# Performance work log

Measured on AMD Instinct MI355X. Metric: run time of the kernel, lower is better.

## Reference

```python
import jax, jax.numpy as jnp
import numpy as np

V = 32000; D = 512; H = 8; DH = D // H; L = 12; E = 8; FF = 2048
B = 2; S = 1024; MAXPOS = 2048
EPS = 1e-6; NEG = -1e9


def _rmsnorm(x, w):
    return x * jax.lax.rsqrt(jnp.mean(x * x, axis=-1, keepdims=True) + EPS) * w


def setup_inputs() -> dict:
    key = jax.random.key(0)
    ks = jax.random.split(key, 10)
    s = 0.02
    n = lambda k, shp: jax.random.normal(k, shp, jnp.float32) * s
    return {
        "input_ids": jax.random.randint(ks[0], (B, S), 0, V),
        "tok_emb": n(ks[1], (V, D)),
        "pos_emb": n(ks[2], (MAXPOS, D)),
        "Wqkv": n(ks[3], (L, D, 3 * D)), "bqkv": jnp.zeros((L, 3 * D), jnp.float32),
        "Wo": n(ks[4], (L, D, D)), "bo": jnp.zeros((L, D), jnp.float32),
        "rW": n(ks[5], (L, D, E)), "rb": jnp.zeros((L, E), jnp.float32),
        "eW1": n(ks[6], (L, E, D, FF)), "eb1": jnp.zeros((L, E, FF), jnp.float32),
        "eW2": n(ks[7], (L, E, FF, D)), "eb2": jnp.zeros((L, E, D), jnp.float32),
        "n1w": jnp.ones((L, D), jnp.float32), "n2w": jnp.ones((L, D), jnp.float32),
        "now": jnp.ones((D,), jnp.float32), "lmW": n(ks[8], (D, V)),
    }


def _forward(input_ids, tok_emb, pos_emb, Wqkv, bqkv, Wo, bo, rW, rb,
             eW1, eb1, eW2, eb2, n1w, n2w, now, lmW):
    x = tok_emb[input_ids] + pos_emb[:S]              # [B,S,D]
    causal = jnp.tril(jnp.ones((S, S), bool))         # lower-triangular mask

    def step(x, p):
        wqkv, bq, wo, bo_, rw, rb_, w1, b1, w2, b2, g1, g2 = p
        # --- causal self-attention ---
        h = _rmsnorm(x, g1)
        qkv = h @ wqkv + bq
        q, k, v = [t.reshape(B, S, H, DH) for t in jnp.split(qkv, 3, axis=-1)]
        scores = jnp.einsum('bqhd,bkhd->bhqk', q, k) / jnp.sqrt(jnp.float32(DH))
        scores = jnp.where(causal, scores, NEG)
        attn = jax.nn.softmax(scores, axis=-1)
        o = jnp.einsum('bhqk,bkhd->bqhd', attn, v).reshape(B, S, D) @ wo + bo_
        x = x + o
        # --- MoE layer, top-1 routing ---
        h = _rmsnorm(x, g2)
        rl = h @ rw + rb_                              # router logits [B,S,E]
        probs = jax.nn.softmax(rl, axis=-1)
        top_w = jnp.max(probs, axis=-1)                # top-1 gate weight [B,S]
        top_i = jnp.argmax(probs, axis=-1)             # expert id [B,S]
        one_hot = jax.nn.one_hot(top_i, E, dtype=x.dtype)
        frac = jnp.mean(one_hot, axis=(0, 1))          # fraction of tokens per expert
        pmean = jnp.mean(probs, axis=(0, 1))           # mean router prob per expert
        aux = E * jnp.sum(frac * pmean)                # switch-style load-balance loss
        disp = (one_hot * top_w[..., None]).reshape(-1, E)   # [T,E] weighted dispatch
        hf = h.reshape(-1, D)                          # [T,D]
        hid = jax.nn.gelu(jnp.einsum('td,edf->etf', hf, w1) + b1[:, None, :], approximate=False)
        outs = jnp.einsum('etf,efd->etd', hid, w2) + b2[:, None, :]
        y = jnp.einsum('etd,te->td', outs, disp).reshape(B, S, D)  # scatter-combine
        x = x + y
        return x, (aux, rl)

    x, (auxes, rlogits) = jax.lax.scan(
        step, x, (Wqkv, bqkv, Wo, bo, rW, rb, eW1, eb1, eW2, eb2, n1w, n2w))
    logits = _rmsnorm(x, now) @ lmW                    # [B,S,V]
    return logits, jnp.sum(auxes), rlogits


def reference(input_ids, tok_emb, pos_emb, Wqkv, bqkv, Wo, bo, rW, rb,
              eW1, eb1, eW2, eb2, n1w, n2w, now, lmW):
    return _forward(input_ids, tok_emb, pos_emb, Wqkv, bqkv, Wo, bo, rW, rb,
                    eW1, eb1, eW2, eb2, n1w, n2w, now, lmW)
```

## Files before the change

kernel.cpp:

```cpp
#include <hip/hip_runtime.h>

constexpr int B_  = 2, S_ = 1024, T_ = 2048;
constexpr int D_  = 512, H_ = 8, DH_ = 64;
constexpr int L_  = 12, E_ = 8, FF_ = 2048;
constexpr int V_  = 32000, D3_ = 1536;

using half8_t = __attribute__((ext_vector_type(8))) _Float16;
using half2_t = __attribute__((ext_vector_type(2))) _Float16;
using f32x4_t = __attribute__((ext_vector_type(4))) float;

__device__ __forceinline__ float wred(float v){
#pragma unroll
  for (int off = 32; off; off >>= 1) v += __shfl_xor(v, off);
  return v;
}
__device__ __forceinline__ float gelu_f(float v){
  return 0.5f * v * (1.f + erff(v * 0.70710678118654752f));
}

__global__ void k_embed(const int* __restrict__ ids, const float* __restrict__ tok,
                        const float* __restrict__ pos, float* __restrict__ x){
  int t = blockIdx.x;
  int s = t & (S_ - 1);
  int id = ids[t];
  const float* tr = tok + (size_t)id * D_;
  const float* pr = pos + (size_t)s  * D_;
  float* xr = x + (size_t)t * D_;
  for (int d = threadIdx.x; d < D_; d += blockDim.x) xr[d] = tr[d] + pr[d];
}

__global__ __launch_bounds__(64) void k_norm_router(
    const float* __restrict__ x, const float* __restrict__ nw,
    const float* __restrict__ rW, const float* __restrict__ rb,
    float* __restrict__ h, float* __restrict__ rl_out,
    float* __restrict__ topw, int* __restrict__ topi){
  const int t = blockIdx.x, lane = threadIdx.x;
  const float* xr = x + (size_t)t * D_;
  const float4 xv0 = *reinterpret_cast<const float4*>(xr + (lane << 2));
  const float4 xv1 = *reinterpret_cast<const float4*>(xr + 256 + (lane << 2));
  float ss = xv0.x*xv0.x + xv0.y*xv0.y + xv0.z*xv0.z + xv0.w*xv0.w
           + xv1.x*xv1.x + xv1.y*xv1.y + xv1.z*xv1.z + xv1.w*xv1.w;
  ss = wred(ss);
  const float sc = rsqrtf(ss * (1.f / (float)D_) + 1e-6f);
  const float4 w0 = *reinterpret_cast<const float4*>(nw + (lane << 2));
  const float4 w1 = *reinterpret_cast<const float4*>(nw + 256 + (lane << 2));
  float hv[8];
  hv[0] = xv0.x*sc*w0.x; hv[1] = xv0.y*sc*w0.y; hv[2] = xv0.z*sc*w0.z; hv[3] = xv0.w*sc*w0.w;
  hv[4] = xv1.x*sc*w1.x; hv[5] = xv1.y*sc*w1.y; hv[6] = xv1.z*sc*w1.z; hv[7] = xv1.w*sc*w1.w;
  float* hr = h + (size_t)t * D_;
  *reinterpret_cast<float4*>(hr + (lane << 2))       = make_float4(hv[0], hv[1], hv[2], hv[3]);
  *reinterpret_cast<float4*>(hr + 256 + (lane << 2)) = make_float4(hv[4], hv[5], hv[6], hv[7]);
  float acc[8] = {0,0,0,0,0,0,0,0};
#pragma unroll
  for (int u = 0; u < 8; u++){
    const int d = (u < 4) ? ((lane << 2) + u) : (256 + (lane << 2) + u - 4);
    const float4 ra = *reinterpret_cast<const float4*>(rW + (size_t)d * E_);
    const float4 rb4 = *reinterpret_cast<const float4*>(rW + (size_t)d * E_ + 4);
    acc[0] += hv[u]*ra.x;  acc[1] += hv[u]*ra.y;  acc[2] += hv[u]*ra.z;  acc[3] += hv[u]*ra.w;
    acc[4] += hv[u]*rb4.x; acc[5] += hv[u]*rb4.y; acc[6] += hv[u]*rb4.z; acc[7] += hv[u]*rb4.w;
  }
  float rl[8];
#pragma unroll
  for (int e = 0; e < 8; e++) rl[e] = wred(acc[e]) + rb[e];
  float mx = rl[0];
#pragma unroll
  for (int e = 1; e < 8; e++) mx = fmaxf(mx, rl[e]);
  float p[8], s = 0.f;
#pragma unroll
  for (int e = 0; e < 8; e++){ p[e] = __expf(rl[e] - mx); s += p[e]; }
  const float inv = 1.f / s;
  int arg = 0; float best = rl[0];
#pragma unroll
  for (int e = 1; e < 8; e++) if (rl[e] > best){ best = rl[e]; arg = e; }
  if (lane == 0){
#pragma unroll
    for (int e = 0; e < 8; e++) rl_out[(size_t)t * E_ + e] = rl[e];
    topw[t] = p[arg] * inv;
    topi[t] = arg;
  }
}

__global__ __launch_bounds__(1024) void k_route_scan2(
    const int* __restrict__ topi, const float* __restrict__ rl,
    int* __restrict__ seg, int* __restrict__ perm, float* __restrict__ aux){
  __shared__ int cnt[8], segs[9], cur[8];
  __shared__ float psums[8];
  const int tid = threadIdx.x;
  if (tid < 8){ cnt[tid] = 0; psums[tid] = 0.f; }
  __syncthreads();
  const int t0 = tid, t1 = tid + 1024;
  const int e0 = topi[t0], e1 = topi[t1];
  atomicAdd(&cnt[e0], 1);
  atomicAdd(&cnt[e1], 1);
  float ps[8] = {0,0,0,0,0,0,0,0};
#pragma unroll
  for (int k = 0; k < 2; k++){
    const float* r = rl + (size_t)(k ? t1 : t0) * E_;
    float v[8];
#pragma unroll
    for (int e = 0; e < 8; e++) v[e] = r[e];
    float mx = v[0];
#pragma unroll
    for (int e = 1; e < 8; e++) mx = fmaxf(mx, v[e]);
    float s = 0.f;
#pragma unroll
    for (int e = 0; e < 8; e++){ v[e] = __expf(v[e] - mx); s += v[e]; }
    const float is = 1.f / s;
#pragma unroll
    for (int e = 0; e < 8; e++) ps[e] += v[e] * is;
  }
#pragma unroll
  for (int e = 0; e < 8; e++) ps[e] = wred(ps[e]);
  if ((tid & 63) == 0){
#pragma unroll
    for (int e = 0; e < 8; e++) atomicAdd(&psums[e], ps[e]);
  }
  __syncthreads();
  if (tid == 0){
    segs[0] = 0;
#pragma unroll
    for (int e = 0; e < 8; e++) segs[e + 1] = segs[e] + cnt[e];
#pragma unroll
    for (int e = 0; e < 8; e++) cur[e] = segs[e];
  }
  __syncthreads();
  if (tid < 9) seg[tid] = segs[tid];
  const int p0 = atomicAdd(&cur[e0], 1); perm[p0] = t0;
  const int p1 = atomicAdd(&cur[e1], 1); perm[p1] = t1;
  if (tid == 0){
    float av = 0.f;
#pragma unroll
    for (int e = 0; e < 8; e++) av += (float)cnt[e] * psums[e];
    aux[0] += 8.f * av * (1.f / ((float)T_ * (float)T_));
  }
}

template<int BM, int BN, int NPROD, int EPI, bool MOE, bool APERM, int SWZROWS, bool ANORM>
__global__ __launch_bounds__(256) void k_mgemm(
    const float* __restrict__ A, const float* __restrict__ Bm,
    const float* __restrict__ bias, float* __restrict__ C,
    int M, int N, int K,
    const int* __restrict__ seg, const int* __restrict__ perm,
    const float* __restrict__ topw, const float* __restrict__ nw){
  constexpr int FM = BM / 32, FN = BN / 32;
  const int tid = threadIdx.x;
  int rowTile, colTile;
  if (SWZROWS > 0){
    const int nwg = gridDim.x;
    const int bid = blockIdx.x;
    const int lb = (bid & 7) * (nwg >> 3) + (bid >> 3);
    rowTile = lb % SWZROWS;
    colTile = lb / SWZROWS;
  } else {
    colTile = blockIdx.x; rowTile = blockIdx.y;
  }
  int e = 0, s0 = 0, cnt = M;
  if (MOE){ e = blockIdx.z; s0 = seg[e]; cnt = seg[e + 1] - s0; }
  const int row0 = rowTile * BM, col0 = colTile * BN;
  if (MOE && row0 >= cnt) return;
  const float* Bp = Bm + (size_t)e * K * N;
  const float* bp = bias + (size_t)e * N;

  __shared__ __align__(16) _Float16 Ah[BM * 32];
  __shared__ __align__(16) _Float16 Al[NPROD == 3 ? BM * 32 : 8];
  __shared__ __align__(16) _Float16 Bh[BN * 32];
  __shared__ __align__(16) _Float16 Bl[NPROD == 3 ? BN * 32 : 8];

  const int am = (BM == 64) ? (tid >> 2) : (tid >> 1);
  const int agrow = row0 + am;
  const bool aval = agrow < cnt;
  const float* Arow = nullptr;
  if (aval){
    int ridx = APERM ? perm[s0 + agrow] : (MOE ? s0 + agrow : agrow);
    Arow = A + (size_t)ridx * K;
  }
  const int asub = am >> 4;
  const int cb = (BN == 128) ? ((tid & 31) << 2) : ((tid & 15) << 2);
  const int p0 = (BN == 128) ? (tid >> 5) : (tid >> 4);
  constexpr int NBI = (BN == 128) ? 2 : 1;

  const int lane = tid & 63, w = tid >> 6;
  const int wm0 = (w >> 1) * (BM / 2), wn0 = (w & 1) * (BN / 2);

  float ascale = 1.f;
  if (ANORM){
    float ss = 0.f;
    if (BM == 64){
      const int kg = tid & 3;
      for (int k0 = 0; k0 < K; k0 += 32){
        const float4 a0 = *reinterpret_cast<const float4*>(Arow + k0 + (kg << 3));
        const float4 a1 = *reinterpret_cast<const float4*>(Arow + k0 + (kg << 3) + 4);
        ss += a0.x*a0.x + a0.y*a0.y + a0.z*a0.z + a0.w*a0.w
            + a1.x*a1.x + a1.y*a1.y + a1.z*a1.z + a1.w*a1.w;
      }
      ss += __shfl_xor(ss, 1);
      ss += __shfl_xor(ss, 2);
    } else {
      const int kgb = (tid & 1) << 1;
      for (int k0 = 0; k0 < K; k0 += 32){
#pragma unroll
        for (int kq = 0; kq < 2; kq++){
          const int kg = kgb + kq;
          const float4 a0 = *reinterpret_cast<const float4*>(Arow + k0 + (kg << 3));
          const float4 a1 = *reinterpret_cast<const float4*>(Arow + k0 + (kg << 3) + 4);
          ss += a0.x*a0.x + a0.y*a0.y + a0.z*a0.z + a0.w*a0.w
              + a1.x*a1.x + a1.y*a1.y + a1.z*a1.z + a1.w*a1.w;
        }
      }
      ss += __shfl_xor(ss, 1);
    }
    ascale = rsqrtf(ss * (1.f / (float)K) + 1e-6f);
  }

  f32x4_t acc_hh[FM][FN];
  f32x4_t acc_mx[NPROD == 3 ? FM : 1][NPROD == 3 ? FN : 1];
#pragma unroll
  for (int i = 0; i < FM; i++)
#pragma unroll
    for (int j = 0; j < FN; j++){
      acc_hh[i][j] = (f32x4_t){0.f, 0.f, 0.f, 0.f};
      if (NPROD == 3) acc_mx[i][j] = (f32x4_t){0.f, 0.f, 0.f, 0.f};
    }

  for (int k0 = 0; k0 < K; k0 += 32){
    if (BM == 64){
      const int kg = tid & 3;
      float4 av0 = make_float4(0,0,0,0), av1 = make_float4(0,0,0,0);
      if (aval){
        av0 = *reinterpret_cast<const float4*>(Arow + k0 + (kg << 3));
        av1 = *reinterpret_cast<const float4*>(Arow + k0 + (kg << 3) + 4);
      }
      float a8[8] = {av0.x, av0.y, av0.z, av0.w, av1.x, av1.y, av1.z, av1.w};
      if (ANORM){
        const float4 w0 = *reinterpret_cast<const float4*>(nw + k0 + (kg << 3));
        const float4 w1 = *reinterpret_cast<const float4*>(nw + k0 + (kg << 3) + 4);
        const float wn8[8] = {w0.x, w0.y, w0.z, w0.w, w1.x, w1.y, w1.z, w1.w};
#pragma unroll
        for (int u = 0; u < 8; u++) a8[u] *= ascale * wn8[u];
      }
      half8_t hi, lo;
#pragma unroll
      for (int u = 0; u < 8; u++){
        hi[u] = (_Float16)a8[u];
        if (NPROD == 3) lo[u] = (_Float16)((a8[u] - (float)hi[u]) * 2048.f);
      }
      const int lidx = (am & 15) + (kg << 4);
      const int base = asub * 512 + ((lidx ^ (asub & 7)) << 3);
      *reinterpret_cast<half8_t*>(&Ah[base]) = hi;
      if (NPROD == 3) *reinterpret_cast<half8_t*>(&Al[base]) = lo;
    } else {
      const int kgb = (tid & 1) << 1;
#pragma unroll
      for (int kq = 0; kq < 2; kq++){
        const int kg = kgb + kq;
        float4 av0 = make_float4(0,0,0,0), av1 = make_float4(0,0,0,0);
        if (aval){
          av0 = *reinterpret_cast<const float4*>(Arow + k0 + (kg << 3));
          av1 = *reinterpret_cast<const float4*>(Arow + k0 + (kg << 3) + 4);
        }
        float a8[8] = {av0.x, av0.y, av0.z, av0.w, av1.x, av1.y, av1.z, av1.w};
        if (ANORM){
          const float4 w0 = *reinterpret_cast<const float4*>(nw + k0 + (kg << 3));
          const float4 w1 = *reinterpret_cast<const float4*>(nw + k0 + (kg << 3) + 4);
          const float wn8[8] = {w0.x, w0.y, w0.z, w0.w, w1.x, w1.y, w1.z, w1.w};
#pragma unroll
          for (int u = 0; u < 8; u++) a8[u] *= ascale * wn8[u];
        }
        half8_t hi;
#pragma unroll
        for (int u = 0; u < 8; u++) hi[u] = (_Float16)a8[u];
        const int lidx = (am & 15) + (kg << 4);
        *reinterpret_cast<half8_t*>(&Ah[asub * 512 + ((lidx ^ (asub & 7)) << 3)]) = hi;
      }
    }
#pragma unroll
    for (int it = 0; it < NBI; it++){
      const int kk = ((BN == 128) ? (p0 + (it << 3)) : p0) << 1;
      const int kg = kk >> 3, e2 = kk & 7;
      const float4 b0 = *reinterpret_cast<const float4*>(Bp + (size_t)(k0 + kk) * N + col0 + cb);
      const float4 b1 = *reinterpret_cast<const float4*>(Bp + (size_t)(k0 + kk + 1) * N + col0 + cb);
      const float b0a[4] = {b0.x, b0.y, b0.z, b0.w};
      const float b1a[4] = {b1.x, b1.y, b1.z, b1.w};
#pragma unroll
      for (int j = 0; j < 4; j++){
        const int c = cb + j, sub = c >> 4;
        const int lidx = (c & 15) + (kg << 4);
        const int base = sub * 512 + ((lidx ^ (sub & 7)) << 3) + e2;
        _Float16 h0 = (_Float16)b0a[j], h1 = (_Float16)b1a[j];
        *reinterpret_cast<half2_t*>(&Bh[base]) = (half2_t){h0, h1};
        if (NPROD == 3){
          _Float16 l0 = (_Float16)((b0a[j] - (float)h0) * 2048.f);
          _Float16 l1 = (_Float16)((b1a[j] - (float)h1) * 2048.f);
          *reinterpret_cast<half2_t*>(&Bl[base]) = (half2_t){l0, l1};
        }
      }
    }
    __syncthreads();
    half8_t fAh[FM], fBh[FN];
    half8_t fAl[NPROD == 3 ? FM : 1], fBl[NPROD == 3 ? FN : 1];
#pragma unroll
    for (int fm = 0; fm < FM; fm++){
      const int s = (wm0 >> 4) + fm;
      const int ofs = s * 512 + ((lane ^ (s & 7)) << 3);
      fAh[fm] = *reinterpret_cast<const half8_t*>(&Ah[ofs]);
      if (NPROD == 3) fAl[fm] = *reinterpret_cast<const half8_t*>(&Al[ofs]);
    }
#pragma unroll
    for (int fn = 0; fn < FN; fn++){
      const int s = (wn0 >> 4) + fn;
      const int ofs = s * 512 + ((lane ^ (s & 7)) << 3);
      fBh[fn] = *reinterpret_cast<const half8_t*>(&Bh[ofs]);
      if (NPROD == 3) fBl[fn] = *reinterpret_cast<const half8_t*>(&Bl[ofs]);
    }
#pragma unroll
    for (int fm = 0; fm < FM; fm++)
#pragma unroll
      for (int fn = 0; fn < FN; fn++){
        acc_hh[fm][fn] = __builtin_amdgcn_mfma_f32_16x16x32_f16(
            fAh[fm], fBh[fn], acc_hh[fm][fn], 0, 0, 0);
        if (NPROD == 3){
          acc_mx[fm][fn] = __builtin_amdgcn_mfma_f32_16x16x32_f16(
              fAh[fm], fBl[fn], acc_mx[fm][fn], 0, 0, 0);
          acc_mx[fm][fn] = __builtin_amdgcn_mfma_f32_16x16x32_f16(
              fAl[fm], fBh[fn], acc_mx[fm][fn], 0, 0, 0);
        }
      }
    __syncthreads();
  }

  const int lr = lane & 15, kg4 = lane >> 4;
#pragma unroll
  for (int fm = 0; fm < FM; fm++){
#pragma unroll
    for (int reg = 0; reg < 4; reg++){
      const int grow = row0 + wm0 + fm * 16 + (kg4 << 2) + reg;
      if (grow >= cnt) continue;
      int trow = 0; float tw = 0.f;
      if (EPI == 3){ trow = perm[s0 + grow]; tw = topw[trow]; }
#pragma unroll
      for (int fn = 0; fn < FN; fn++){
        const int col = col0 + wn0 + fn * 16 + lr;
        float v = acc_hh[fm][fn][reg];
        if (NPROD == 3) v += acc_mx[fm][fn][reg] * (1.f / 2048.f);
        if (EPI == 0){
          C[(size_t)grow * N + col] = v + bp[col];
        } else if (EPI == 1){
          C[(size_t)grow * N + col] += v + bp[col];
        } else if (EPI == 2){
          C[(size_t)(s0 + grow) * N + col] = gelu_f(v + bp[col]);
        } else if (EPI == 3){
          C[(size_t)trow * N + col] += tw * (v + bp[col]);
        } else {
          C[(size_t)grow * N + col] = v;
        }
      }
    }
  }
}

__global__ __launch_bounds__(256) void k_attn5(const float* __restrict__ qkv,
                                               float* __restrict__ o,
                                               float* __restrict__ attp,
                                               float* __restrict__ attml){
  __shared__ __align__(16) _Float16 Khi[4096], Klo[4096], Vhi[4096], Vlo[4096];
  __shared__ __align__(16) float pbuf[4][16 * 68];
  const int tid = threadIdx.x, w = tid >> 6, lane = tid & 63;
  const int lr = lane & 15, g = lane >> 4;
  const int bid = blockIdx.x;
  int bh, qt, kt0, kt1, mode;
  if (bid < 128){        bh = bid >> 3;            qt = 8 + (bid & 7);  kt0 = 0; kt1 = 7;  mode = 1; }
  else if (bid < 256){   const int j = bid - 128;  bh = j >> 3; qt = 7 - (j & 7);  kt0 = 0; kt1 = qt; mode = 0; }
  else {                 const int j = bid - 256;  bh = j >> 3; qt = 15 - (j & 7); kt0 = 8; kt1 = qt; mode = 2; }
  const int b = bh >> 3, h = bh & 7;
  const size_t bbase = (size_t)(b << 10) * D3_;
  const int hoff = h * 64;
  const int qg = (qt << 6) + (w << 4) + lr;

  half8_t qhi[2], qlo[2];
#pragma unroll
  for (int ks = 0; ks < 2; ks++){
    const float* qp = qkv + bbase + (size_t)qg * D3_ + hoff + ks * 32 + g * 8;
    const float4 f0 = *reinterpret_cast<const float4*>(qp);
    const float4 f1 = *reinterpret_cast<const float4*>(qp + 4);
    const float qa[8] = {f0.x, f0.y, f0.z, f0.w, f1.x, f1.y, f1.z, f1.w};
#pragma unroll
    for (int e = 0; e < 8; e++){
      const float v = qa[e] * 0.125f;
      const _Float16 hi = (_Float16)v;
      qhi[ks][e] = hi;
      qlo[ks][e] = (_Float16)((v - (float)hi) * 2048.f);
    }
  }

  float m = -1e30f, l = 0.f;
  f32x4_t oacc[4];
#pragma unroll
  for (int s = 0; s < 4; s++) oacc[s] = (f32x4_t){0.f, 0.f, 0.f, 0.f};

  const int kK = tid >> 2, quad = tid & 3;
  const int kp = tid >> 3, oct = tid & 7;

  float ka[16], va[8], vb[8];
  auto loadregs = [&](int kt){
    const int j0 = kt << 6;
    const float* kr = qkv + bbase + (size_t)(j0 + kK) * D3_ + 512 + hoff + quad * 16;
    const float4 f0 = *reinterpret_cast<const float4*>(kr);
    const float4 f1 = *reinterpret_cast<const float4*>(kr + 4);
    const float4 f2 = *reinterpret_cast<const float4*>(kr + 8);
    const float4 f3 = *reinterpret_cast<const float4*>(kr + 12);
    ka[0]=f0.x; ka[1]=f0.y; ka[2]=f0.z; ka[3]=f0.w;
    ka[4]=f1.x; ka[5]=f1.y; ka[6]=f1.z; ka[7]=f1.w;
    ka[8]=f2.x; ka[9]=f2.y; ka[10]=f2.z; ka[11]=f2.w;
    ka[12]=f3.x; ka[13]=f3.y; ka[14]=f3.z; ka[15]=f3.w;
    const int k0v = kp << 1;
    const float* vr = qkv + bbase + (size_t)(j0 + k0v) * D3_ + 1024 + hoff + oct * 8;
    const float4 a0 = *reinterpret_cast<const float4*>(vr);
    const float4 a1 = *reinterpret_cast<const float4*>(vr + 4);
    const float4 b0 = *reinterpret_cast<const float4*>(vr + D3_);
    const float4 b1 = *reinterpret_cast<const float4*>(vr + D3_ + 4);
    va[0]=a0.x; va[1]=a0.y; va[2]=a0.z; va[3]=a0.w;
    va[4]=a1.x; va[5]=a1.y; va[6]=a1.z; va[7]=a1.w;
    vb[0]=b0.x; vb[1]=b0.y; vb[2]=b0.z; vb[3]=b0.w;
    vb[4]=b1.x; vb[5]=b1.y; vb[6]=b1.z; vb[7]=b1.w;
  };
  auto writelds = [&](){
    const int ksd = quad >> 1;
#pragma unroll
    for (int ch = 0; ch < 2; ch++){
      const int kgd = ((quad << 1) + ch) & 3;
      const int base = ksd * 2048 + (kK >> 4) * 512 + (((kK & 15) + (kgd << 4)) << 3);
      half8_t hi, lo;
#pragma unroll
      for (int e = 0; e < 8; e++){
        const float v = ka[ch * 8 + e];
        const _Float16 hv = (_Float16)v;
        hi[e] = hv;
        lo[e] = (_Float16)((v - (float)hv) * 2048.f);
      }
      *reinterpret_cast<half8_t*>(&Khi[base]) = hi;
      *reinterpret_cast<half8_t*>(&Klo[base]) = lo;
    }
    const int ksk = kp >> 4, kgk = (kp >> 2) & 3, e0 = (kp & 3) << 1;
#pragma unroll
    for (int j = 0; j < 8; j++){
      const int d = oct * 8 + j;
      const int lidx = (d & 15) + (kgk << 4);
      const int sw = lidx ^ kgk ^ (ksk << 2);
      const int fa = ksk * 2048 + (d >> 4) * 512 + (sw << 3) + e0;
      const _Float16 h0 = (_Float16)va[j], h1 = (_Float16)vb[j];
      *reinterpret_cast<half2_t*>(&Vhi[fa]) = (half2_t){h0, h1};
      const _Float16 l0 = (_Float16)((va[j] - (float)h0) * 2048.f);
      const _Float16 l1 = (_Float16)((vb[j] - (float)h1) * 2048.f);
      *reinterpret_cast<half2_t*>(&Vlo[fa]) = (half2_t){l0, l1};
    }
  };

  loadregs(kt0);
  for (int kt = kt0; kt <= kt1; kt++){
    const int j0 = kt << 6;
    __syncthreads();
    writelds();
    if (kt < kt1) loadregs(kt + 1);
    __syncthreads();

    f32x4_t dfr[4];
#pragma unroll
    for (int s = 0; s < 4; s++){
      f32x4_t acc = (f32x4_t){0.f, 0.f, 0.f, 0.f};
      f32x4_t mix = (f32x4_t){0.f, 0.f, 0.f, 0.f};
#pragma unroll
      for (int ks = 0; ks < 2; ks++){
        const int base = ks * 2048 + s * 512 + lane * 8;
        const half8_t khi = *reinterpret_cast<const half8_t*>(&Khi[base]);
        const half8_t klo = *reinterpret_cast<const half8_t*>(&Klo[base]);
        acc = __builtin_amdgcn_mfma_f32_16x16x32_f16(khi, qhi[ks], acc, 0, 0, 0);
        mix = __builtin_amdgcn_mfma_f32_16x16x32_f16(khi, qlo[ks], mix, 0, 0, 0);
        mix = __builtin_amdgcn_mfma_f32_16x16x32_f16(klo, qhi[ks], mix, 0, 0, 0);
      }
#pragma unroll
      for (int r = 0; r < 4; r++) dfr[s][r] = acc[r] + mix[r] * (1.f / 2048.f);
    }
    if (kt == qt){
#pragma unroll
      for (int s = 0; s < 4; s++)
#pragma unroll
        for (int r = 0; r < 4; r++){
          const int keyg = j0 + (g << 2) + r + (s << 4);
          if (keyg > qg) dfr[s][r] = -1e30f;
        }
    }
    float mloc = dfr[0][0];
#pragma unroll
    for (int s = 0; s < 4; s++)
#pragma unroll
      for (int r = 0; r < 4; r++) mloc = fmaxf(mloc, dfr[s][r]);
    mloc = fmaxf(mloc, __shfl_xor(mloc, 16));
    mloc = fmaxf(mloc, __shfl_xor(mloc, 32));
    const float mn = fmaxf(m, mloc);
    const float cr = __expf(m - mn);
    float psum = 0.f;
#pragma unroll
    for (int s = 0; s < 4; s++)
#pragma unroll
      for (int r = 0; r < 4; r++){
        const float p = __expf(dfr[s][r] - mn);
        psum += p;
        pbuf[w][lr * 68 + (s << 4) + (g << 2) + r] = p;
      }
    psum += __shfl_xor(psum, 16);
    psum += __shfl_xor(psum, 32);
    l = l * cr + psum;
    m = mn;
#pragma unroll
    for (int s = 0; s < 4; s++)
#pragma unroll
      for (int r = 0; r < 4; r++) oacc[s][r] *= cr;

    half8_t phi[2], plo[2];
#pragma unroll
    for (int ks = 0; ks < 2; ks++){
      const float* pp = &pbuf[w][lr * 68 + ks * 32 + g * 8];
      const float4 p0 = *reinterpret_cast<const float4*>(pp);
      const float4 p1 = *reinterpret_cast<const float4*>(pp + 4);
      const float pa[8] = {p0.x,p0.y,p0.z,p0.w, p1.x,p1.y,p1.z,p1.w};
#pragma unroll
      for (int e = 0; e < 8; e++){
        const _Float16 hv = (_Float16)pa[e];
        phi[ks][e] = hv;
        plo[ks][e] = (_Float16)((pa[e] - (float)hv) * 2048.f);
      }
    }
#pragma unroll
    for (int s = 0; s < 4; s++){
      f32x4_t mix = (f32x4_t){0.f, 0.f, 0.f, 0.f};
#pragma unroll
      for (int ks = 0; ks < 2; ks++){
        const int sw = lane ^ g ^ (ks << 2);
        const int base = ks * 2048 + s * 512 + sw * 8;
        const half8_t vhi = *reinterpret_cast<const half8_t*>(&Vhi[base]);
        const half8_t vlo = *reinterpret_cast<const half8_t*>(&Vlo[base]);
        oacc[s] = __builtin_amdgcn_mfma_f32_16x16x32_f16(vhi, phi[ks], oacc[s], 0, 0, 0);
        mix = __builtin_amdgcn_mfma_f32_16x16x32_f16(vhi, plo[ks], mix, 0, 0, 0);
        mix = __builtin_amdgcn_mfma_f32_16x16x32_f16(vlo, phi[ks], mix, 0, 0, 0);
      }
#pragma unroll
      for (int r = 0; r < 4; r++) oacc[s][r] += mix[r] * (1.f / 2048.f);
    }
  }

  if (mode == 0){
    const float linv = 1.f / l;
    float* orow = o + (size_t)((b << 10) + qg) * D_ + hoff;
#pragma unroll
    for (int s = 0; s < 4; s++)
#pragma unroll
      for (int r = 0; r < 4; r++){
        const int d = (g << 2) + r + (s << 4);
        orow[d] = oacc[s][r] * linv;
      }
  } else {
    const int pidx = (((bh << 3) + (qt - 8)) << 1) + (mode - 1);
    float* pO = attp + (size_t)pidx * 4096;
    const int qloc = (w << 4) + lr;
#pragma unroll
    for (int s = 0; s < 4; s++)
#pragma unroll
      for (int r = 0; r < 4; r++){
        const int d = (g << 2) + r + (s << 4);
        pO[qloc * 64 + d] = oacc[s][r];
      }
    if (g == 0){
      attml[pidx * 128 + qloc]      = m;
      attml[pidx * 128 + 64 + qloc] = l;
    }
  }
}

__global__ __launch_bounds__(256) void k_attn_comb(const float* __restrict__ attp,
                                                   const float* __restrict__ attml,
                                                   float* __restrict__ o){
  const int bid = blockIdx.x;
  const int bh = bid >> 3, i = bid & 7, qt = 8 + i;
  const int b = bh >> 3, h = bh & 7;
  const int pidx0 = ((bh << 3) + i) << 1;
  const float* pA = attp + (size_t)pidx0 * 4096;
  const float* pB = pA + 4096;
  const float* mlA = attml + pidx0 * 128;
  const float* mlB = mlA + 128;
  const int tid = threadIdx.x;
  const int q = tid >> 2, dg = (tid & 3) << 4;
  const float mA = mlA[q], lA = mlA[64 + q];
  const float mB = mlB[q], lB = mlB[64 + q];
  const float M = fmaxf(mA, mB);
  const float cA = __expf(mA - M), cB = __expf(mB - M);
  const float linv = 1.f / (lA * cA + lB * cB);
  float* orow = o + (size_t)((b << 10) + (qt << 6) + q) * D_ + h * 64;
#pragma unroll
  for (int j = 0; j < 4; j++){
    const int d = dg + (j << 2);
    const float4 a = *reinterpret_cast<const float4*>(pA + q * 64 + d);
    const float4 bb = *reinterpret_cast<const float4*>(pB + q * 64 + d);
    *reinterpret_cast<float4*>(orow + d) = make_float4(
        (a.x * cA + bb.x * cB) * linv, (a.y * cA + bb.y * cB) * linv,
        (a.z * cA + bb.z * cB) * linv, (a.w * cA + bb.w * cB) * linv);
  }
}

extern "C" void kernel_launch(void* const* d_in, const int* in_sizes, int n_in,
                              void* d_out, int out_size, void* d_ws, size_t ws_size,
                              hipStream_t stream){
  const int*   ids  = (const int*)  d_in[0];
  const float* tok  = (const float*)d_in[1];
  const float* pos  = (const float*)d_in[2];
  const float* Wqkv = (const float*)d_in[3];
  const float* bqkv = (const float*)d_in[4];
  const float* Wo   = (const float*)d_in[5];
  const float* bo   = (const float*)d_in[6];
  const float* rW   = (const float*)d_in[7];
  const float* rb   = (const float*)d_in[8];
  const float* eW1  = (const float*)d_in[9];
  const float* eb1  = (const float*)d_in[10];
  const float* eW2  = (const float*)d_in[11];
  const float* eb2  = (const float*)d_in[12];
  const float* n1w  = (const float*)d_in[13];
  const float* n2w  = (const float*)d_in[14];
  const float* noww = (const float*)d_in[15];
  const float* lmW  = (const float*)d_in[16];

  float* out    = (float*)d_out;
  float* logits = out;
  float* aux    = out + (size_t)T_ * V_;
  float* rlog   = aux + 1;

  float* ws = (float*)d_ws;
  size_t off = 0;
  float* x     = ws + off; off += (size_t)T_ * D_;
  float* h     = ws + off; off += (size_t)T_ * D_;
  float* qkv   = ws + off; off += (size_t)T_ * D3_;
  float* attno = ws + off; off += (size_t)T_ * D_;
  float* hid   = ws + off; off += (size_t)T_ * FF_;
  float* topw  = ws + off; off += T_;
  int* topi    = (int*)(ws + off); off += T_;
  int* perm    = (int*)(ws + off); off += T_;
  int* seg     = (int*)(ws + off); off += (E_ + 1);
  float* attp  = ws + off; off += 16 * 8 * 2 * 4096;
  float* attml = ws + off; off += 16 * 8 * 2 * 128;

  hipMemsetAsync(aux, 0, sizeof(float), stream);
  k_embed<<<T_, 256, 0, stream>>>(ids, tok, pos, x);

  for (int l = 0; l < L_; l++){
    k_mgemm<64, 128, 3, 0, false, false, 0, true><<<dim3(D3_ / 128, T_ / 64), 256, 0, stream>>>(
        x, Wqkv + (size_t)l * D_ * D3_, bqkv + (size_t)l * D3_, qkv,
        T_, D3_, D_, seg, perm, topw, n1w + (size_t)l * D_);
    k_attn5<<<384, 256, 0, stream>>>(qkv, attno, attp, attml);
    k_attn_comb<<<128, 256, 0, stream>>>(attp, attml, attno);
    k_mgemm<64, 64, 3, 1, false, false, 0, false><<<dim3(D_ / 64, T_ / 64), 256, 0, stream>>>(
        attno, Wo + (size_t)l * D_ * D_, bo + (size_t)l * D_, x,
        T_, D_, D_, seg, perm, topw, nullptr);
    k_norm_router<<<T_, 64, 0, stream>>>(x, n2w + (size_t)l * D_,
        rW + (size_t)l * D_ * E_, rb + (size_t)l * E_,
        h, rlog + (size_t)l * T_ * E_, topw, topi);
    k_route_scan2<<<1, 1024, 0, stream>>>(topi, rlog + (size_t)l * T_ * E_, seg, perm, aux);
    k_mgemm<64, 128, 3, 2, true, true, 0, false><<<dim3(FF_ / 128, T_ / 64, E_), 256, 0, stream>>>(
        h, eW1 + (size_t)l * E_ * D_ * FF_, eb1 + (size_t)l * E_ * FF_, hid,
        T_, FF_, D_, seg, perm, topw, nullptr);
    k_mgemm<64, 64, 3, 3, true, false, 0, false><<<dim3(D_ / 64, T_ / 64, E_), 256, 0, stream>>>(
        hid, eW2 + (size_t)l * E_ * FF_ * D_, eb2 + (size_t)l * E_ * D_, x,
        T_, D_, FF_, seg, perm, topw, nullptr);
  }

  k_mgemm<128, 128, 1, 4, false, false, 16, true><<<(T_ / 128) * (V_ / 128), 256, 0, stream>>>(
      x, lmW, nullptr, logits, T_, V_, D_, seg, perm, topw, noww);
}
```

Before: 3.164 ms.

## Double-buffer MFMA GEMM shared tiles with register prefetch of next K slice

The generic MFMA GEMM kernel now double-buffers its A and B shared-memory tiles. The next K slice is loaded into registers before the MFMAs on the current slice run, then converted and stored to the other buffer, which drops one barrier per iteration. The B loads are also restructured: each thread gathers 8 consecutive K rows of one column and writes a full half8 vector, replacing the old half2 scattered stores. This costs twice the LDS and more registers, which may lower occupancy, and the B global loads become scalar strided reads instead of float4.

Result: slower. 3.670 ms (+16.0%).

```diff
diff --git a/kernel.cpp b/kernel.cpp
--- a/kernel.cpp
+++ b/kernel.cpp
@@ -143,6 +143,8 @@
     const int* __restrict__ seg, const int* __restrict__ perm,
     const float* __restrict__ topw, const float* __restrict__ nw){
   constexpr int FM = BM / 32, FN = BN / 32;
+  constexpr int BSLOTS = BN / 64;
+  constexpr int AREG = (BM == 64) ? 8 : 16;
   const int tid = threadIdx.x;
   int rowTile, colTile;
   if (SWZROWS > 0){
@@ -161,10 +163,10 @@
   const float* Bp = Bm + (size_t)e * K * N;
   const float* bp = bias + (size_t)e * N;
 
-  __shared__ __align__(16) _Float16 Ah[BM * 32];
-  __shared__ __align__(16) _Float16 Al[NPROD == 3 ? BM * 32 : 8];
-  __shared__ __align__(16) _Float16 Bh[BN * 32];
-  __shared__ __align__(16) _Float16 Bl[NPROD == 3 ? BN * 32 : 8];
+  __shared__ __align__(16) _Float16 Ah[2][BM * 32];
+  __shared__ __align__(16) _Float16 Al[NPROD == 3 ? 2 : 1][NPROD == 3 ? BM * 32 : 8];
+  __shared__ __align__(16) _Float16 Bh[2][BN * 32];
+  __shared__ __align__(16) _Float16 Bl[NPROD == 3 ? 2 : 1][NPROD == 3 ? BN * 32 : 8];
 
   const int am = (BM == 64) ? (tid >> 2) : (tid >> 1);
   const int agrow = row0 + am;
@@ -175,9 +177,6 @@
     Arow = A + (size_t)ridx * K;
   }
   const int asub = am >> 4;
-  const int cb = (BN == 128) ? ((tid & 31) << 2) : ((tid & 15) << 2);
-  const int p0 = (BN == 128) ? (tid >> 5) : (tid >> 4);
-  constexpr int NBI = (BN == 128) ? 2 : 1;
 
   const int lane = tid & 63, w = tid >> 6;
   const int wm0 = (w >> 1) * (BM / 2), wn0 = (w & 1) * (BN / 2);
@@ -212,6 +211,110 @@
     ascale = rsqrtf(ss * (1.f / (float)K) + 1e-6f);
   }
 
+  float areg[AREG], wreg[ANORM ? AREG : 1], breg[BSLOTS * 8];
+
+  auto aload = [&](int k0){
+    if (BM == 64){
+      const int kg = tid & 3;
+      float4 a0 = make_float4(0,0,0,0), a1 = make_float4(0,0,0,0);
+      if (aval){
+        a0 = *reinterpret_cast<const float4*>(Arow + k0 + (kg << 3));
+        a1 = *reinterpret_cast<const float4*>(Arow + k0 + (kg << 3) + 4);
+      }
+      areg[0]=a0.x; areg[1]=a0.y; areg[2]=a0.z; areg[3]=a0.w;
+      areg[4]=a1.x; areg[5]=a1.y; areg[6]=a1.z; areg[7]=a1.w;
+      if (ANORM){
+        const float4 w0v = *reinterpret_cast<const float4*>(nw + k0 + (kg << 3));
+        const float4 w1v = *reinterpret_cast<const float4*>(nw + k0 + (kg << 3) + 4);
+        wreg[0]=w0v.x; wreg[1]=w0v.y; wreg[2]=w0v.z; wreg[3]=w0v.w;
+        wreg[4]=w1v.x; wreg[5]=w1v.y; wreg[6]=w1v.z; wreg[7]=w1v.w;
+      }
+    } else {
+      const int kgb = (tid & 1) << 1;
+#pragma unroll
+      for (int kq = 0; kq < 2; kq++){
+        const int kg = kgb + kq;
+        float4 a0 = make_float4(0,0,0,0), a1 = make_float4(0,0,0,0);
+        if (aval){
+          a0 = *reinterpret_cast<const float4*>(Arow + k0 + (kg << 3));
+          a1 = *reinterpret_cast<const float4*>(Arow + k0 + (kg << 3) + 4);
+        }
+        areg[kq*8+0]=a0.x; areg[kq*8+1]=a0.y; areg[kq*8+2]=a0.z; areg[kq*8+3]=a0.w;
+        areg[kq*8+4]=a1.x; areg[kq*8+5]=a1.y; areg[kq*8+6]=a1.z; areg[kq*8+7]=a1.w;
+        if (ANORM){
+          const float4 w0v = *reinterpret_cast<const float4*>(nw + k0 + (kg << 3));
+          const float4 w1v = *reinterpret_cast<const float4*>(nw + k0 + (kg << 3) + 4);
+          wreg[kq*8+0]=w0v.x; wreg[kq*8+1]=w0v.y; wreg[kq*8+2]=w0v.z; wreg[kq*8+3]=w0v.w;
+          wreg[kq*8+4]=w1v.x; wreg[kq*8+5]=w1v.y; wreg[kq*8+6]=w1v.z; wreg[kq*8+7]=w1v.w;
+        }
+      }
+    }
+  };
+  auto bload = [&](int k0){
+#pragma unroll
+    for (int s = 0; s < BSLOTS; s++){
+      const int sid = s * 256 + tid;
+      const int col = sid & (BN - 1);
+      const int kg  = sid / BN;
+      const float* bpp = Bp + (size_t)(k0 + (kg << 3)) * N + col0 + col;
+#pragma unroll
+      for (int ee = 0; ee < 8; ee++) breg[s*8+ee] = bpp[(size_t)ee * N];
+    }
+  };
+  auto astore = [&](int buf){
+    if (BM == 64){
+      const int kg = tid & 3;
+      half8_t hi, lo;
+#pragma unroll
+      for (int u = 0; u < 8; u++){
+        const float v = ANORM ? areg[u] * ascale * wreg[u] : areg[u];
+        hi[u] = (_Float16)v;
+        if (NPROD == 3) lo[u] = (_Float16)((v - (float)hi[u]) * 2048.f);
+      }
+      const int lidx = (am & 15) + (kg << 4);
+      const int base = asub * 512 + ((lidx ^ (asub & 7)) << 3);
+      *reinterpret_cast<half8_t*>(&Ah[buf][base]) = hi;
+      if (NPROD == 3) *reinterpret_cast<half8_t*>(&Al[buf][base]) = lo;
+    } else {
+      const int kgb = (tid & 1) << 1;
+#pragma unroll
+      for (int kq = 0; kq < 2; kq++){
+        const int kg = kgb + kq;
+        half8_t hi, lo;
+#pragma unroll
+        for (int u = 0; u < 8; u++){
+          const float v = ANORM ? areg[kq*8+u] * ascale * wreg[kq*8+u] : areg[kq*8+u];
+          hi[u] = (_Float16)v;
+          if (NPROD == 3) lo[u] = (_Float16)((v - (float)hi[u]) * 2048.f);
+        }
+        const int lidx = (am & 15) + (kg << 4);
+        const int base = asub * 512 + ((lidx ^ (asub & 7)) << 3);
+        *reinterpret_cast<half8_t*>(&Ah[buf][base]) = hi;
+        if (NPROD == 3) *reinterpret_cast<half8_t*>(&Al[buf][base]) = lo;
+      }
+    }
+  };
+  auto bstore = [&](int buf){
+#pragma unroll
+    for (int s = 0; s < BSLOTS; s++){
+      const int sid = s * 256 + tid;
+      const int col = sid & (BN - 1);
+      const int kg  = sid / BN;
+      half8_t hi, lo;
+#pragma unroll
+      for (int ee = 0; ee < 8; ee++){
+        const float v = breg[s*8+ee];
+        hi[ee] = (_Float16)v;
+        if (NPROD == 3) lo[ee] = (_Float16)((v - (float)hi[ee]) * 2048.f);
+      }
+      const int sub = col >> 4;
+      const int lidx = (col & 15) + (kg << 4);
+      const int base = sub * 512 + ((lidx ^ (sub & 7)) << 3);
+      *reinterpret_cast<half8_t*>(&Bh[buf][base]) = hi;
+      if (NPROD == 3) *reinterpret_cast<half8_t*>(&Bl[buf][base]) = lo;
+    }
+  };
+
   f32x4_t acc_hh[FM][FN];
   f32x4_t acc_mx[NPROD == 3 ? FM : 1][NPROD == 3 ? FN : 1];
 #pragma unroll
@@ -222,95 +325,29 @@
       if (NPROD == 3) acc_mx[i][j] = (f32x4_t){0.f, 0.f, 0.f, 0.f};
     }
 
+  aload(0); bload(0);
+  astore(0); bstore(0);
+  __syncthreads();
+  int cur = 0;
+
   for (int k0 = 0; k0 < K; k0 += 32){
-    if (BM == 64){
-      const int kg = tid & 3;
-      float4 av0 = make_float4(0,0,0,0), av1 = make_float4(0,0,0,0);
-      if (aval){
-        av0 = *reinterpret_cast<const float4*>(Arow + k0 + (kg << 3));
-        av1 = *reinterpret_cast<const float4*>(Arow + k0 + (kg << 3) + 4);
-      }
-      float a8[8] = {av0.x, av0.y, av0.z, av0.w, av1.x, av1.y, av1.z, av1.w};
-      if (ANORM){
-        const float4 w0 = *reinterpret_cast<const float4*>(nw + k0 + (kg << 3));
-        const float4 w1 = *reinterpret_cast<const float4*>(nw + k0 + (kg << 3) + 4);
-        const float wn8[8] = {w0.x, w0.y, w0.z, w0.w, w1.x, w1.y, w1.z, w1.w};
-#pragma unroll
-        for (int u = 0; u < 8; u++) a8[u] *= ascale * wn8[u];
-      }
-      half8_t hi, lo;
-#pragma unroll
-      for (int u = 0; u < 8; u++){
-        hi[u] = (_Float16)a8[u];
-        if (NPROD == 3) lo[u] = (_Float16)((a8[u] - (float)hi[u]) * 2048.f);
-      }
-      const int lidx = (am & 15) + (kg << 4);
-      const int base = asub * 512 + ((lidx ^ (asub & 7)) << 3);
-      *reinterpret_cast<half8_t*>(&Ah[base]) = hi;
-      if (NPROD == 3) *reinterpret_cast<half8_t*>(&Al[base]) = lo;
-    } else {
-      const int kgb = (tid & 1) << 1;
-#pragma unroll
-      for (int kq = 0; kq < 2; kq++){
-        const int kg = kgb + kq;
-        float4 av0 = make_float4(0,0,0,0), av1 = make_float4(0,0,0,0);
-        if (aval){
-          av0 = *reinterpret_cast<const float4*>(Arow + k0 + (kg << 3));
-          av1 = *reinterpret_cast<const float4*>(Arow + k0 + (kg << 3) + 4);
-        }
-        float a8[8] = {av0.x, av0.y, av0.z, av0.w, av1.x, av1.y, av1.z, av1.w};
-        if (ANORM){
-          const float4 w0 = *reinterpret_cast<const float4*>(nw + k0 + (kg << 3));
-          const float4 w1 = *reinterpret_cast<const float4*>(nw + k0 + (kg << 3) + 4);
-          const float wn8[8] = {w0.x, w0.y, w0.z, w0.w, w1.x, w1.y, w1.z, w1.w};
-#pragma unroll
-          for (int u = 0; u < 8; u++) a8[u] *= ascale * wn8[u];
-        }
-        half8_t hi;
-#pragma unroll
-        for (int u = 0; u < 8; u++) hi[u] = (_Float16)a8[u];
-        const int lidx = (am & 15) + (kg << 4);
-        *reinterpret_cast<half8_t*>(&Ah[asub * 512 + ((lidx ^ (asub & 7)) << 3)]) = hi;
-      }
-    }
-#pragma unroll
-    for (int it = 0; it < NBI; it++){
-      const int kk = ((BN == 128) ? (p0 + (it << 3)) : p0) << 1;
-      const int kg = kk >> 3, e2 = kk & 7;
-      const float4 b0 = *reinterpret_cast<const float4*>(Bp + (size_t)(k0 + kk) * N + col0 + cb);
-      const float4 b1 = *reinterpret_cast<const float4*>(Bp + (size_t)(k0 + kk + 1) * N + col0 + cb);
-      const float b0a[4] = {b0.x, b0.y, b0.z, b0.w};
-      const float b1a[4] = {b1.x, b1.y, b1.z, b1.w};
-#pragma unroll
-      for (int j = 0; j < 4; j++){
-        const int c = cb + j, sub = c >> 4;
-        const int lidx = (c & 15) + (kg << 4);
-        const int base = sub * 512 + ((lidx ^ (sub & 7)) << 3) + e2;
-        _Float16 h0 = (_Float16)b0a[j], h1 = (_Float16)b1a[j];
-        *reinterpret_cast<half2_t*>(&Bh[base]) = (half2_t){h0, h1};
-        if (NPROD == 3){
-          _Float16 l0 = (_Float16)((b0a[j] - (float)h0) * 2048.f);
-          _Float16 l1 = (_Float16)((b1a[j] - (float)h1) * 2048.f);
-          *reinterpret_cast<half2_t*>(&Bl[base]) = (half2_t){l0, l1};
-        }
-      }
-    }
-    __syncthreads();
+    const bool hasNext = (k0 + 32 < K);
+    if (hasNext){ aload(k0 + 32); bload(k0 + 32); }
     half8_t fAh[FM], fBh[FN];
     half8_t fAl[NPROD == 3 ? FM : 1], fBl[NPROD == 3 ? FN : 1];
 #pragma unroll
     for (int fm = 0; fm < FM; fm++){
       const int s = (wm0 >> 4) + fm;
       const int ofs = s * 512 + ((lane ^ (s & 7)) << 3);
-      fAh[fm] = *reinterpret_cast<const half8_t*>(&Ah[ofs]);
-      if (NPROD == 3) fAl[fm] = *reinterpret_cast<const half8_t*>(&Al[ofs]);
+      fAh[fm] = *reinterpret_cast<const half8_t*>(&Ah[cur][ofs]);
+      if (NPROD == 3) fAl[fm] = *reinterpret_cast<const half8_t*>(&Al[cur][ofs]);
     }
 #pragma unroll
     for (int fn = 0; fn < FN; fn++){
       const int s = (wn0 >> 4) + fn;
       const int ofs = s * 512 + ((lane ^ (s & 7)) << 3);
-      fBh[fn] = *reinterpret_cast<const half8_t*>(&Bh[ofs]);
-      if (NPROD == 3) fBl[fn] = *reinterpret_cast<const half8_t*>(&Bl[ofs]);
+      fBh[fn] = *reinterpret_cast<const half8_t*>(&Bh[cur][ofs]);
+      if (NPROD == 3) fBl[fn] = *reinterpret_cast<const half8_t*>(&Bl[cur][ofs]);
     }
 #pragma unroll
     for (int fm = 0; fm < FM; fm++)
@@ -325,7 +362,11 @@
               fAl[fm], fBh[fn], acc_mx[fm][fn], 0, 0, 0);
         }
       }
-    __syncthreads();
+    if (hasNext){
+      astore(cur ^ 1); bstore(cur ^ 1);
+      __syncthreads();
+      cur ^= 1;
+    }
   }
 
   const int lr = lane & 15, kg4 = lane >> 4;
```
